# Optimization experiments

Hardware: AMD Instinct MI355X
Metric: run time of the kernel (lower is better)

The kernel has to match this reference:

```python
import jax, jax.numpy as jnp
import numpy as np

# pywt 'db4' decomposition low-pass filter (L = 8 taps)
_DEC_LO = np.array([
    -0.010597401784997278, 0.032883011666982945, 0.030841381835986965,
    -0.18703481171888114, -0.02798376941698385, 0.6308807679295904,
    0.7148465705525415, 0.23037781330885523], dtype=np.float32)
# pywt convention: dec_hi[n] = (-1)^(n+1) * dec_lo[L-1-n]
_SIGNS = np.array([-1.0, 1.0] * 4, dtype=np.float32)
_DEC_HI = _DEC_LO[::-1].copy() * _SIGNS

DEC_LO = jnp.asarray(_DEC_LO)
DEC_HI = jnp.asarray(_DEC_HI)
LEVELS = 3


def _dwt_per(x):
    """One level of periodization-mode DWT along axis 1.

    x: (B, N, F) with N even. Returns (cA, cD), each (B, N//2, F).
    Matches pywt: c[k] = sum_j f[j] * x[(2k + 1 - j) mod N].
    """
    N = x.shape[1]
    L = DEC_LO.shape[0]
    k = jnp.arange(N // 2)
    j = jnp.arange(L)
    idx = (2 * k[:, None] + 1 - j[None, :]) % N          # (N//2, L)
    g = x[:, idx, :]                                      # (B, N//2, L, F)
    cA = jnp.einsum('bklf,l->bkf', g, DEC_LO)
    cD = jnp.einsum('bklf,l->bkf', g, DEC_HI)
    return cA, cD


def reference(x):
    """Multilevel db4 wavedec (periodization) along axis -2 of (B, N, F).

    Returns the flat coefficient tensor (B, K, F) with pywt ordering
    [cA_L, cD_L, cD_{L-1}, ..., cD_1] concatenated along axis 1.
    """
    a = x
    details = []
    for _ in range(LEVELS):
        a, d = _dwt_per(a)
        details.append(d)
    return jnp.concatenate([a] + details[::-1], axis=1)


def setup_inputs() -> dict:
    key = jax.random.key(0)
    x = jax.random.normal(key, (64, 4096, 64), dtype=jnp.float32)
    return {"x": x}


if __name__ == "__main__":
    out = reference(**setup_inputs())
    print(out.shape)
```

## Files before the change

### kernel.cpp

```cpp
#include <hip/hip_runtime.h>


__device__ __forceinline__ float2 ld2(const float* p) {
    return *reinterpret_cast<const float2*>(p);
}
__device__ __forceinline__ void st2(float* p, float2 v) {
    *reinterpret_cast<float2*>(p) = v;
}
__device__ __forceinline__ float2 fma2(float2 a, float s, float2 c) {
    c.x = fmaf(a.x, s, c.x);
    c.y = fmaf(a.y, s, c.y);
    return c;
}

__global__ __launch_bounds__(256, 2) void dwt3_fused_v4(
    const float* __restrict__ in,
    float* __restrict__ out)
{
    const float LOR[8] = { 0.23037781330885523f,   0.7148465705525415f,
                           0.6308807679295904f,   -0.02798376941698385f,
                          -0.18703481171888114f,   0.030841381835986965f,
                           0.032883011666982945f, -0.010597401784997278f};
    const float HIR[8] = {-0.010597401784997278f, -0.032883011666982945f,
                           0.030841381835986965f,  0.18703481171888114f,
                          -0.02798376941698385f,  -0.6308807679295904f,
                           0.7148465705525415f,   -0.23037781330885523f};

    const int bid  = blockIdx.x;
    const int swz  = (bid & 7) * 64 + (bid >> 3);

    const int lane = threadIdx.x & 63;
    const int wv   = threadIdx.x >> 6;
    const int f    = (lane & 31) * 2;
    const int tsub = lane >> 5;
    const int b    = swz >> 3;
    const int tile = (swz & 7) * 8 + wv * 2 + tsub;
    const int K3   = tile * 8;

    const float* inB  = in  + (size_t)b * 4096 * 64 + f;
    float*       outB = out + (size_t)b * 4096 * 64 + f;

    const int i1s   = 4 * K3 - 18;
    const int tbase = 2 * i1s - 6;

    float2 bufA[16], bufB[16], bufC[16], bufD[10];

    #define ISSUE(BUF, C, N)                                                  \
        _Pragma("unroll")                                                     \
        for (int j = 0; j < (N); ++j) {                                       \
            BUF[j] = ld2(inB + (size_t)((tbase + 16 * (C) + j) & 4095) * 64); \
        }

    ISSUE(bufA, 0, 16)
    ISSUE(bufB, 1, 16)
    ISSUE(bufC, 2, 16)

    float2 w0[8], w1[8], w2[8];
    #pragma unroll
    for (int m = 0; m < 8; ++m) {
        w1[m] = make_float2(0.f, 0.f);
        w2[m] = make_float2(0.f, 0.f);
    }
    #pragma unroll
    for (int m = 0; m < 8; ++m) w0[m] = bufA[m];

    #define STEP(S, X0, X1) {                                                  \
        const int i1 = i1s + (S);                                              \
        _Pragma("unroll")                                                      \
        for (int m = 0; m < 6; ++m) w0[m] = w0[m + 2];                         \
        w0[6] = (X0); w0[7] = (X1);                                            \
        float2 a1 = make_float2(0.f, 0.f);                                     \
        _Pragma("unroll")                                                      \
        for (int m = 0; m < 8; ++m) a1 = fma2(w0[m], LOR[m], a1);              \
        if ((S) >= 18) {                                                       \
            float2 d1 = make_float2(0.f, 0.f);                                 \
            _Pragma("unroll")                                                  \
            for (int m = 0; m < 8; ++m) d1 = fma2(w0[m], HIR[m], d1);          \
            st2(outB + (size_t)((2048 + i1) & 4095) * 64, d1);                 \
        }                                                                      \
        _Pragma("unroll")                                                      \
        for (int m = 0; m < 7; ++m) w1[m] = w1[m + 1];                         \
        w1[7] = a1;                                                            \
        if (((S) & 1) && (S) >= 7) {                                           \
            const int i2 = 2 * K3 + ((S) - 19) / 2;                            \
            float2 a2 = make_float2(0.f, 0.f);                                 \
            _Pragma("unroll")                                                  \
            for (int m = 0; m < 8; ++m) a2 = fma2(w1[m], LOR[m], a2);          \
            if ((S) >= 19) {                                                   \
                float2 d2 = make_float2(0.f, 0.f);                             \
                _Pragma("unroll")                                              \
                for (int m = 0; m < 8; ++m) d2 = fma2(w1[m], HIR[m], d2);      \
                st2(outB + (size_t)((1024 + i2) & 4095) * 64, d2);             \
            }                                                                  \
            _Pragma("unroll")                                                  \
            for (int m = 0; m < 7; ++m) w2[m] = w2[m + 1];                     \
            w2[7] = a2;                                                        \
            if ((S) >= 21 && (((S) - 21) & 3) == 0) {                          \
                const int i3 = K3 + ((S) - 21) / 4;                            \
                float2 a3 = make_float2(0.f, 0.f);                             \
                float2 d3 = make_float2(0.f, 0.f);                             \
                _Pragma("unroll")                                              \
                for (int m = 0; m < 8; ++m) {                                  \
                    a3 = fma2(w2[m], LOR[m], a3);                              \
                    d3 = fma2(w2[m], HIR[m], d3);                              \
                }                                                              \
                st2(outB + (size_t)(i3 & 4095) * 64,         a3);              \
                st2(outB + (size_t)((512 + i3) & 4095) * 64, d3);              \
            }                                                                  \
        }                                                                      \
    }

    {
        float2 a1 = make_float2(0.f, 0.f);
        #pragma unroll
        for (int m = 0; m < 8; ++m) a1 = fma2(w0[m], LOR[m], a1);
        #pragma unroll
        for (int m = 0; m < 7; ++m) w1[m] = w1[m + 1];
        w1[7] = a1;
    }

    #pragma unroll
    for (int s = 1; s <= 4; ++s) STEP(s, bufA[2 * s + 6], bufA[2 * s + 7])

    ISSUE(bufA, 3, 16)
    #pragma unroll
    for (int s = 5; s <= 12; ++s) STEP(s, bufB[2 * s + 6 - 16], bufB[2 * s + 7 - 16])

    ISSUE(bufB, 4, 16)
    #pragma unroll
    for (int s = 13; s <= 20; ++s) STEP(s, bufC[2 * s + 6 - 32], bufC[2 * s + 7 - 32])

    ISSUE(bufC, 5, 16)
    #pragma unroll
    for (int s = 21; s <= 28; ++s) STEP(s, bufA[2 * s + 6 - 48], bufA[2 * s + 7 - 48])

    ISSUE(bufD, 6, 10)
    #pragma unroll
    for (int s = 29; s <= 36; ++s) STEP(s, bufB[2 * s + 6 - 64], bufB[2 * s + 7 - 64])

    #pragma unroll
    for (int s = 37; s <= 44; ++s) STEP(s, bufC[2 * s + 6 - 80], bufC[2 * s + 7 - 80])

    #pragma unroll
    for (int s = 45; s <= 49; ++s) STEP(s, bufD[2 * s + 6 - 96], bufD[2 * s + 7 - 96])

    #undef STEP
    #undef ISSUE
}

extern "C" void kernel_launch(void* const* d_in, const int* in_sizes, int n_in,
                              void* d_out, int out_size, void* d_ws, size_t ws_size,
                              hipStream_t stream) {
    (void)in_sizes; (void)n_in; (void)out_size; (void)d_ws; (void)ws_size;
    const float* x = (const float*)d_in[0];
    float* out = (float*)d_out;
    dwt3_fused_v4<<<512, 256, 0, stream>>>(x, out);
}
```

Measured before the change: 117.2 us.

## Widen per-thread tiles to 32 level-3 outputs with scalar feature lanes

Each thread now handles one feature column with scalar loads instead of float2 pairs. It also produces 32 level-3 coefficients instead of 8, which shrinks the redundant halo reads per tile. The grid is halved to 256 blocks, launch bounds drop to 1 block per SM, and load buffers grow to 32 entries each. The cost is much higher register pressure, fewer wavefronts to hide latency, and narrower memory transactions, while the wrap masks on output stores are dropped.

```diff
diff --git a/kernel.cpp b/kernel.cpp
--- a/kernel.cpp
+++ b/kernel.cpp
@@ -1,19 +1,7 @@
 #include <hip/hip_runtime.h>
 
 
-__device__ __forceinline__ float2 ld2(const float* p) {
-    return *reinterpret_cast<const float2*>(p);
-}
-__device__ __forceinline__ void st2(float* p, float2 v) {
-    *reinterpret_cast<float2*>(p) = v;
-}
-__device__ __forceinline__ float2 fma2(float2 a, float s, float2 c) {
-    c.x = fmaf(a.x, s, c.x);
-    c.y = fmaf(a.y, s, c.y);
-    return c;
-}
-
-__global__ __launch_bounds__(256, 2) void dwt3_fused_v4(
+__global__ __launch_bounds__(256, 1) void dwt3_fused_v7(
     const float* __restrict__ in,
     float* __restrict__ out)
 {
@@ -27,15 +15,13 @@
                            0.7148465705525415f,   -0.23037781330885523f};
 
     const int bid  = blockIdx.x;
-    const int swz  = (bid & 7) * 64 + (bid >> 3);
+    const int swz  = (bid & 7) * 32 + (bid >> 3);
 
-    const int lane = threadIdx.x & 63;
+    const int f    = threadIdx.x & 63;
     const int wv   = threadIdx.x >> 6;
-    const int f    = (lane & 31) * 2;
-    const int tsub = lane >> 5;
-    const int b    = swz >> 3;
-    const int tile = (swz & 7) * 8 + wv * 2 + tsub;
-    const int K3   = tile * 8;
+    const int b    = swz >> 2;
+    const int tile = (swz & 3) * 4 + wv;
+    const int K3   = tile * 32;
 
     const float* inB  = in  + (size_t)b * 4096 * 64 + f;
     float*       outB = out + (size_t)b * 4096 * 64 + f;
@@ -43,24 +29,21 @@
     const int i1s   = 4 * K3 - 18;
     const int tbase = 2 * i1s - 6;
 
-    float2 bufA[16], bufB[16], bufC[16], bufD[10];
+    float bufA[32], bufB[32], bufC[32], bufD[10];
 
-    #define ISSUE(BUF, C, N)                                                  \
-        _Pragma("unroll")                                                     \
-        for (int j = 0; j < (N); ++j) {                                       \
-            BUF[j] = ld2(inB + (size_t)((tbase + 16 * (C) + j) & 4095) * 64); \
+    #define ISSUE(BUF, C, N)                                                    \
+        _Pragma("unroll")                                                       \
+        for (int j = 0; j < (N); ++j) {                                         \
+            BUF[j] = inB[(size_t)((tbase + 32 * (C) + j) & 4095) * 64];         \
         }
 
-    ISSUE(bufA, 0, 16)
-    ISSUE(bufB, 1, 16)
-    ISSUE(bufC, 2, 16)
+    ISSUE(bufA, 0, 32)
+    ISSUE(bufB, 1, 32)
+    ISSUE(bufC, 2, 32)
 
-    float2 w0[8], w1[8], w2[8];
-    #pragma unroll
-    for (int m = 0; m < 8; ++m) {
-        w1[m] = make_float2(0.f, 0.f);
-        w2[m] = make_float2(0.f, 0.f);
-    }
+    float w0[8];
+    float w1[8] = {0,0,0,0,0,0,0,0};
+    float w2[8] = {0,0,0,0,0,0,0,0};
     #pragma unroll
     for (int m = 0; m < 8; ++m) w0[m] = bufA[m];
 
@@ -69,80 +52,91 @@
         _Pragma("unroll")                                                      \
         for (int m = 0; m < 6; ++m) w0[m] = w0[m + 2];                         \
         w0[6] = (X0); w0[7] = (X1);                                            \
-        float2 a1 = make_float2(0.f, 0.f);                                     \
+        float a1 = 0.f;                                                        \
         _Pragma("unroll")                                                      \
-        for (int m = 0; m < 8; ++m) a1 = fma2(w0[m], LOR[m], a1);              \
+        for (int m = 0; m < 8; ++m) a1 = fmaf(w0[m], LOR[m], a1);              \
         if ((S) >= 18) {                                                       \
-            float2 d1 = make_float2(0.f, 0.f);                                 \
+            float d1 = 0.f;                                                    \
             _Pragma("unroll")                                                  \
-            for (int m = 0; m < 8; ++m) d1 = fma2(w0[m], HIR[m], d1);          \
-            st2(outB + (size_t)((2048 + i1) & 4095) * 64, d1);                 \
+            for (int m = 0; m < 8; ++m) d1 = fmaf(w0[m], HIR[m], d1);          \
+            outB[(size_t)(2048 + i1) * 64] = d1;                               \
         }                                                                      \
         _Pragma("unroll")                                                      \
         for (int m = 0; m < 7; ++m) w1[m] = w1[m + 1];                         \
         w1[7] = a1;                                                            \
         if (((S) & 1) && (S) >= 7) {                                           \
             const int i2 = 2 * K3 + ((S) - 19) / 2;                            \
-            float2 a2 = make_float2(0.f, 0.f);                                 \
+            float a2 = 0.f;                                                    \
             _Pragma("unroll")                                                  \
-            for (int m = 0; m < 8; ++m) a2 = fma2(w1[m], LOR[m], a2);          \
+            for (int m = 0; m < 8; ++m) a2 = fmaf(w1[m], LOR[m], a2);          \
             if ((S) >= 19) {                                                   \
-                float2 d2 = make_float2(0.f, 0.f);                             \
+                float d2 = 0.f;                                                \
                 _Pragma("unroll")                                              \
-                for (int m = 0; m < 8; ++m) d2 = fma2(w1[m], HIR[m], d2);      \
-                st2(outB + (size_t)((1024 + i2) & 4095) * 64, d2);             \
+                for (int m = 0; m < 8; ++m) d2 = fmaf(w1[m], HIR[m], d2);      \
+                outB[(size_t)(1024 + i2) * 64] = d2;                           \
             }                                                                  \
             _Pragma("unroll")                                                  \
             for (int m = 0; m < 7; ++m) w2[m] = w2[m + 1];                     \
             w2[7] = a2;                                                        \
             if ((S) >= 21 && (((S) - 21) & 3) == 0) {                          \
                 const int i3 = K3 + ((S) - 21) / 4;                            \
-                float2 a3 = make_float2(0.f, 0.f);                             \
-                float2 d3 = make_float2(0.f, 0.f);                             \
+                float a3 = 0.f, d3 = 0.f;                                      \
                 _Pragma("unroll")                                              \
                 for (int m = 0; m < 8; ++m) {                                  \
-                    a3 = fma2(w2[m], LOR[m], a3);                              \
-                    d3 = fma2(w2[m], HIR[m], d3);                              \
+                    a3 = fmaf(w2[m], LOR[m], a3);                              \
+                    d3 = fmaf(w2[m], HIR[m], d3);                              \
                 }                                                              \
-                st2(outB + (size_t)(i3 & 4095) * 64,         a3);              \
-                st2(outB + (size_t)((512 + i3) & 4095) * 64, d3);              \
+                outB[(size_t)i3 * 64]         = a3;                            \
+                outB[(size_t)(512 + i3) * 64] = d3;                            \
             }                                                                  \
         }                                                                      \
     }
 
     {
-        float2 a1 = make_float2(0.f, 0.f);
+        float a1 = 0.f;
         #pragma unroll
-        for (int m = 0; m < 8; ++m) a1 = fma2(w0[m], LOR[m], a1);
+        for (int m = 0; m < 8; ++m) a1 = fmaf(w0[m], LOR[m], a1);
         #pragma unroll
         for (int m = 0; m < 7; ++m) w1[m] = w1[m + 1];
         w1[7] = a1;
     }
 
     #pragma unroll
-    for (int s = 1; s <= 4; ++s) STEP(s, bufA[2 * s + 6], bufA[2 * s + 7])
+    for (int s = 1; s <= 12; ++s) STEP(s, bufA[2 * s + 6], bufA[2 * s + 7])
 
-    ISSUE(bufA, 3, 16)
+    ISSUE(bufA, 3, 32)
     #pragma unroll
-    for (int s = 5; s <= 12; ++s) STEP(s, bufB[2 * s + 6 - 16], bufB[2 * s + 7 - 16])
+    for (int s = 13; s <= 28; ++s) STEP(s, bufB[2 * s + 6 - 32], bufB[2 * s + 7 - 32])
 
-    ISSUE(bufB, 4, 16)
+    ISSUE(bufB, 4, 32)
     #pragma unroll
-    for (int s = 13; s <= 20; ++s) STEP(s, bufC[2 * s + 6 - 32], bufC[2 * s + 7 - 32])
+    for (int s = 29; s <= 44; ++s) STEP(s, bufC[2 * s + 6 - 64], bufC[2 * s + 7 - 64])
 
-    ISSUE(bufC, 5, 16)
+    ISSUE(bufC, 5, 32)
     #pragma unroll
-    for (int s = 21; s <= 28; ++s) STEP(s, bufA[2 * s + 6 - 48], bufA[2 * s + 7 - 48])
+    for (int s = 45; s <= 60; ++s) STEP(s, bufA[2 * s + 6 - 96], bufA[2 * s + 7 - 96])
 
-    ISSUE(bufD, 6, 10)
+    ISSUE(bufA, 6, 32)
     #pragma unroll
-    for (int s = 29; s <= 36; ++s) STEP(s, bufB[2 * s + 6 - 64], bufB[2 * s + 7 - 64])
+    for (int s = 61; s <= 76; ++s) STEP(s, bufB[2 * s + 6 - 128], bufB[2 * s + 7 - 128])
+
+    ISSUE(bufB, 7, 32)
+    #pragma unroll
+    for (int s = 77; s <= 92; ++s) STEP(s, bufC[2 * s + 6 - 160], bufC[2 * s + 7 - 160])
+
+    ISSUE(bufC, 8, 32)
+    #pragma unroll
+    for (int s = 93; s <= 108; ++s) STEP(s, bufA[2 * s + 6 - 192], bufA[2 * s + 7 - 192])
+
+    ISSUE(bufD, 9, 10)
+    #pragma unroll
+    for (int s = 109; s <= 124; ++s) STEP(s, bufB[2 * s + 6 - 224], bufB[2 * s + 7 - 224])
 
     #pragma unroll
-    for (int s = 37; s <= 44; ++s) STEP(s, bufC[2 * s + 6 - 80], bufC[2 * s + 7 - 80])
+    for (int s = 125; s <= 140; ++s) STEP(s, bufC[2 * s + 6 - 256], bufC[2 * s + 7 - 256])
 
     #pragma unroll
-    for (int s = 45; s <= 49; ++s) STEP(s, bufD[2 * s + 6 - 96], bufD[2 * s + 7 - 96])
+    for (int s = 141; s <= 145; ++s) STEP(s, bufD[2 * s + 6 - 288], bufD[2 * s + 7 - 288])
 
     #undef STEP
     #undef ISSUE
@@ -154,5 +148,5 @@
     (void)in_sizes; (void)n_in; (void)out_size; (void)d_ws; (void)ws_size;
     const float* x = (const float*)d_in[0];
     float* out = (float*)d_out;
-    dwt3_fused_v4<<<512, 256, 0, stream>>>(x, out);
+    dwt3_fused_v7<<<256, 256, 0, stream>>>(x, out);
 }
```

Result: no change. 117.3 us (+0.0%).
